# Kernel optimization log

Hardware: AMD Instinct MI355X
Metric: run time of the kernel (lower is better)

The kernel has to match this reference:

```python
import jax, jax.numpy as jnp
import numpy as np

N_TOKENS = 8192
IN_F = 4096
OUT_F = 4096
QMIN, QMAX = -128, 127  # get_quantized_range(8)
IN_SCALE = 0.02
OUT_SCALE = 0.05
IN_ZP = 0
OUT_ZP = 0


def setup_inputs() -> dict:
    key = jax.random.key(0)
    k1, k2, k3, k4 = jax.random.split(key, 4)
    x = jax.random.randint(k1, (N_TOKENS, IN_F), QMIN, QMAX + 1, dtype=jnp.int8)
    weight = jax.random.randint(k2, (OUT_F, IN_F), QMIN, QMAX + 1, dtype=jnp.int8)
    bias = jax.random.randint(k3, (OUT_F,), -1000, 1001, dtype=jnp.int32)
    weight_scale = jax.random.uniform(k4, (OUT_F, 1), dtype=jnp.float32, minval=0.005, maxval=0.02)
    return {"x": x, "weight": weight, "bias": bias, "weight_scale": weight_scale}


def reference(x, weight, bias, weight_scale):
    # int32-accumulated GEMM: [N, in] @ [in, out] + bias  (CPU path of the torch module)
    acc = jnp.matmul(x.astype(jnp.int32), weight.T.astype(jnp.int32)) + bias  # [N, out] int32
    ws = jnp.swapaxes(weight_scale, -1, -2)  # [1, out] per-output-channel scale
    out = acc.astype(jnp.float32) * (IN_SCALE * ws / OUT_SCALE)
    out = out + OUT_ZP
    out = jnp.clip(jnp.round(out), QMIN, QMAX).astype(jnp.int8)
    return out
```

## Files before the change

kernel.cpp:

```cpp
#include <hip/hip_runtime.h>
#include <hip/hip_bf16.h>
#include <stdint.h>

#define N_TOKENS 8192
#define IN_F 4096
#define OUT_F 4096

#define BM 256
#define BN 256
#define BKB 64
#define NKT (IN_F / BKB)

typedef int int32x4 __attribute__((ext_vector_type(4)));

__device__ __forceinline__ void gload_lds16(const signed char* g, signed char* lds) {
  __builtin_amdgcn_global_load_lds(
      (const __attribute__((address_space(1))) void*)g,
      (__attribute__((address_space(3))) void*)lds, 16, 0, 0);
}

__global__ void pack_kernel(const int4* __restrict__ xs, const int4* __restrict__ ws,
                            uchar4* __restrict__ xd, uchar4* __restrict__ wd,
                            int n4x, int n4tot) {
  const int stride = gridDim.x * blockDim.x;
  for (int i = blockIdx.x * blockDim.x + threadIdx.x; i < n4tot; i += stride) {
    int4 v;
    if (i < n4x) v = xs[i];
    else v = ws[i - n4x];
    uchar4 p;
    p.x = (unsigned char)(v.x & 255);
    p.y = (unsigned char)(v.y & 255);
    p.z = (unsigned char)(v.z & 255);
    p.w = (unsigned char)(v.w & 255);
    if (i < n4x) xd[i] = p;
    else wd[i - n4x] = p;
  }
}

__global__ __launch_bounds__(512, 2) void gemm_i8(
    const signed char* __restrict__ A, const signed char* __restrict__ B,
    const int* __restrict__ bias, const float* __restrict__ wscale,
    int* __restrict__ out) {
  __shared__ __align__(16) signed char sA[3][BM * BKB];
  __shared__ __align__(16) signed char sB[3][BN * BKB];

  const int tid = threadIdx.x;
  const int lane = tid & 63;
  const int w = tid >> 6;
  const int wr = w >> 2;
  const int wc = w & 3;

  const int brow = blockIdx.y * BM;
  const int bcol = blockIdx.x * BN;

  const int csrc = (((lane & 3) ^ ((lane >> 3) & 3)) << 4);
  const int r0 = w * 16 + (lane >> 2);
  const signed char* gA0 = A + (size_t)(brow + r0) * IN_F + csrc;
  const signed char* gB0 = B + (size_t)(bcol + r0) * IN_F + csrc;
  const int ldst = w * 1024 + lane * 16;

#define STAGE(tt, bf)                                                  \
  do {                                                                 \
    const size_t ko = (size_t)(tt)*BKB;                                \
    gload_lds16(gA0 + ko, &sA[bf][ldst]);                              \
    gload_lds16(gA0 + ko + (size_t)128 * IN_F, &sA[bf][ldst + 8192]);  \
    gload_lds16(gB0 + ko, &sB[bf][ldst]);                              \
    gload_lds16(gB0 + ko + (size_t)128 * IN_F, &sB[bf][ldst + 8192]);  \
  } while (0)

  const int cfrag = (((lane >> 4) ^ ((lane >> 1) & 3)) << 4);
  const int aoff = (wr * 128 + (lane & 15)) * BKB + cfrag;
  const int boff = (wc * 64 + (lane & 15)) * BKB + cfrag;

  int32x4 acc[8][4];
#pragma unroll
  for (int m = 0; m < 8; ++m)
#pragma unroll
    for (int n = 0; n < 4; ++n) acc[m][n] = (int32x4){0, 0, 0, 0};

  STAGE(0, 0);
  STAGE(1, 1);
  asm volatile("s_waitcnt vmcnt(4)" ::: "memory");
  __builtin_amdgcn_s_barrier();

  int bufR = 0, bufS = 2;
  for (int t = 0; t < NKT; ++t) {
    if (t < NKT - 2) STAGE(t + 2, bufS);

    int32x4 a[8], b[4];
#pragma unroll
    for (int n = 0; n < 4; ++n) b[n] = *(const int32x4*)&sB[bufR][boff + n * 1024];
#pragma unroll
    for (int m = 0; m < 4; ++m) a[m] = *(const int32x4*)&sA[bufR][aoff + m * 1024];
    __builtin_amdgcn_s_setprio(1);
#pragma unroll
    for (int m = 0; m < 4; ++m)
#pragma unroll
      for (int n = 0; n < 4; ++n)
        acc[m][n] = __builtin_amdgcn_mfma_i32_16x16x64_i8(a[m], b[n], acc[m][n], 0, 0, 0);
    __builtin_amdgcn_s_setprio(0);
    __builtin_amdgcn_s_barrier();
#pragma unroll
    for (int m = 4; m < 8; ++m) a[m] = *(const int32x4*)&sA[bufR][aoff + m * 1024];
    __builtin_amdgcn_s_setprio(1);
#pragma unroll
    for (int m = 4; m < 8; ++m)
#pragma unroll
      for (int n = 0; n < 4; ++n)
        acc[m][n] = __builtin_amdgcn_mfma_i32_16x16x64_i8(a[m], b[n], acc[m][n], 0, 0, 0);
    __builtin_amdgcn_s_setprio(0);

    if (t < NKT - 2) {
      asm volatile("s_waitcnt vmcnt(4) lgkmcnt(0)" ::: "memory");
      __builtin_amdgcn_s_barrier();
    } else if (t == NKT - 2) {
      asm volatile("s_waitcnt vmcnt(0) lgkmcnt(0)" ::: "memory");
      __builtin_amdgcn_s_barrier();
    }
    bufR = (bufR == 2) ? 0 : bufR + 1;
    bufS = (bufS == 2) ? 0 : bufS + 1;
  }
#undef STAGE

  const int colb = bcol + wc * 64 + (lane & 15);
  const int rowb = brow + wr * 128 + ((lane >> 4) << 2);
#pragma unroll
  for (int n = 0; n < 4; ++n) {
    const int col = colb + n * 16;
    const float s = 0.02f * wscale[col] / 0.05f;
    const int bz = bias[col];
#pragma unroll
    for (int m = 0; m < 8; ++m) {
      const int row0 = rowb + m * 16;
#pragma unroll
      for (int r = 0; r < 4; ++r) {
        float f = (float)(acc[m][n][r] + bz) * s;
        f = rintf(f);
        f = fminf(127.f, fmaxf(-128.f, f));
        out[(size_t)(row0 + r) * OUT_F + col] = (int)f;
      }
    }
  }
}

extern "C" void kernel_launch(void* const* d_in, const int* in_sizes, int n_in,
                              void* d_out, int out_size, void* d_ws, size_t ws_size,
                              hipStream_t stream) {
  const int* x = (const int*)d_in[0];
  const int* w = (const int*)d_in[1];
  const int* bias = (const int*)d_in[2];
  const float* wsc = (const float*)d_in[3];
  int* out = (int*)d_out;

  signed char* xp = (signed char*)d_ws;
  signed char* wp = xp + (size_t)N_TOKENS * IN_F;

  const int n4x = N_TOKENS * IN_F / 4;
  const int n4w = OUT_F * IN_F / 4;
  const int n4tot = n4x + n4w;

  pack_kernel<<<2048, 256, 0, stream>>>((const int4*)x, (const int4*)w,
                                        (uchar4*)xp, (uchar4*)wp, n4x, n4tot);

  dim3 grid(OUT_F / BN, N_TOKENS / BM);
  gemm_i8<<<grid, dim3(512), 0, stream>>>(xp, wp, bias, wsc, out);
}
```

Baseline: 442.0 us.

## Double K tile to 128 with two-buffer, four-phase interleaved load/MFMA pipeline

Raises the K tile from 64 to 128 bytes and replaces the triple-buffered LDS ring with double buffering. Each K iteration now runs four MFMA phases. The next tile's global-to-LDS loads are spread across those phases, and fine-grained vmcnt waits make sure each half of the tile is resident before it is read. This halves the number of loop iterations and spreads memory traffic between compute bursts. In exchange it adds more barriers per iteration, raises LDS use to 128KB, and the changed XOR swizzle and single prefetch stage may leave load latency less hidden.

```diff
diff --git a/kernel.cpp b/kernel.cpp
--- a/kernel.cpp
+++ b/kernel.cpp
@@ -8,7 +8,7 @@
 
 #define BM 256
 #define BN 256
-#define BKB 64
+#define BKB 128
 #define NKT (IN_F / BKB)
 
 typedef int int32x4 __attribute__((ext_vector_type(4)));
@@ -41,8 +41,8 @@
     const signed char* __restrict__ A, const signed char* __restrict__ B,
     const int* __restrict__ bias, const float* __restrict__ wscale,
     int* __restrict__ out) {
-  __shared__ __align__(16) signed char sA[3][BM * BKB];
-  __shared__ __align__(16) signed char sB[3][BN * BKB];
+  __shared__ __align__(16) signed char sA[2][BM * BKB];
+  __shared__ __align__(16) signed char sB[2][BN * BKB];
 
   const int tid = threadIdx.x;
   const int lane = tid & 63;
@@ -53,24 +53,17 @@
   const int brow = blockIdx.y * BM;
   const int bcol = blockIdx.x * BN;
 
-  const int csrc = (((lane & 3) ^ ((lane >> 3) & 3)) << 4);
-  const int r0 = w * 16 + (lane >> 2);
-  const signed char* gA0 = A + (size_t)(brow + r0) * IN_F + csrc;
-  const signed char* gB0 = B + (size_t)(bcol + r0) * IN_F + csrc;
-  const int ldst = w * 1024 + lane * 16;
-
-#define STAGE(tt, bf)                                                  \
-  do {                                                                 \
-    const size_t ko = (size_t)(tt)*BKB;                                \
-    gload_lds16(gA0 + ko, &sA[bf][ldst]);                              \
-    gload_lds16(gA0 + ko + (size_t)128 * IN_F, &sA[bf][ldst + 8192]);  \
-    gload_lds16(gB0 + ko, &sB[bf][ldst]);                              \
-    gload_lds16(gB0 + ko + (size_t)128 * IN_F, &sB[bf][ldst + 8192]);  \
-  } while (0)
-
-  const int cfrag = (((lane >> 4) ^ ((lane >> 1) & 3)) << 4);
-  const int aoff = (wr * 128 + (lane & 15)) * BKB + cfrag;
-  const int boff = (wc * 64 + (lane & 15)) * BKB + cfrag;
+  const int grow = tid >> 3;
+  const int gchk = ((tid & 7) ^ (grow & 7)) << 4;
+  const signed char* gA = A + (size_t)(brow + grow) * IN_F + gchk;
+  const signed char* gB = B + (size_t)(bcol + grow) * IN_F + gchk;
+  const int lst = tid << 4;
+#define GSTR ((size_t)64 * IN_F)
+
+  const int c0 = (((lane >> 4) ^ (lane & 7)) << 4);
+  const int c1 = c0 ^ 64;
+  const int rA = (wr * 128 + (lane & 15)) * BKB;
+  const int rB = (wc * 64 + (lane & 15)) * BKB;
 
   int32x4 acc[8][4];
 #pragma unroll
@@ -78,20 +71,32 @@
 #pragma unroll
     for (int n = 0; n < 4; ++n) acc[m][n] = (int32x4){0, 0, 0, 0};
 
-  STAGE(0, 0);
-  STAGE(1, 1);
-  asm volatile("s_waitcnt vmcnt(4)" ::: "memory");
+#pragma unroll
+  for (int i = 0; i < 4; ++i) {
+    gload_lds16(gB + i * GSTR, &sB[0][i * 8192 + lst]);
+    gload_lds16(gA + i * GSTR, &sA[0][i * 8192 + lst]);
+  }
+  asm volatile("s_waitcnt vmcnt(0)" ::: "memory");
   __builtin_amdgcn_s_barrier();
 
-  int bufR = 0, bufS = 2;
   for (int t = 0; t < NKT; ++t) {
-    if (t < NKT - 2) STAGE(t + 2, bufS);
-
-    int32x4 a[8], b[4];
-#pragma unroll
-    for (int n = 0; n < 4; ++n) b[n] = *(const int32x4*)&sB[bufR][boff + n * 1024];
-#pragma unroll
-    for (int m = 0; m < 4; ++m) a[m] = *(const int32x4*)&sA[bufR][aoff + m * 1024];
+    const int buf = t & 1;
+    const int nb = buf ^ 1;
+    const bool pf = (t < NKT - 1);
+    const signed char* srcA = gA + (size_t)(t + 1) * BKB;
+    const signed char* srcB = gB + (size_t)(t + 1) * BKB;
+    signed char* dA = &sA[nb][lst];
+    signed char* dB = &sB[nb][lst];
+    int32x4 a[4], b[4];
+
+#pragma unroll
+    for (int n = 0; n < 4; ++n) b[n] = *(const int32x4*)&sB[buf][rB + n * 2048 + c0];
+#pragma unroll
+    for (int m = 0; m < 4; ++m) a[m] = *(const int32x4*)&sA[buf][rA + m * 2048 + c0];
+    if (pf) { gload_lds16(srcB, dB); gload_lds16(srcB + 2 * GSTR, dB + 16384); }
+    __builtin_amdgcn_s_barrier();
+    asm volatile("s_waitcnt lgkmcnt(0)" ::: "memory");
+    __builtin_amdgcn_sched_barrier(0);
     __builtin_amdgcn_s_setprio(1);
 #pragma unroll
     for (int m = 0; m < 4; ++m)
@@ -99,28 +104,59 @@
       for (int n = 0; n < 4; ++n)
         acc[m][n] = __builtin_amdgcn_mfma_i32_16x16x64_i8(a[m], b[n], acc[m][n], 0, 0, 0);
     __builtin_amdgcn_s_setprio(0);
-    __builtin_amdgcn_s_barrier();
-#pragma unroll
-    for (int m = 4; m < 8; ++m) a[m] = *(const int32x4*)&sA[bufR][aoff + m * 1024];
-    __builtin_amdgcn_s_setprio(1);
-#pragma unroll
-    for (int m = 4; m < 8; ++m)
+    if (pf) asm volatile("s_waitcnt vmcnt(2)" ::: "memory");
+    else    asm volatile("s_waitcnt vmcnt(0)" ::: "memory");
+    __builtin_amdgcn_s_barrier();
+
+#pragma unroll
+    for (int m = 0; m < 4; ++m) a[m] = *(const int32x4*)&sA[buf][rA + (m + 4) * 2048 + c0];
+    if (pf) { gload_lds16(srcB + GSTR, dB + 8192); gload_lds16(srcB + 3 * GSTR, dB + 24576); }
+    __builtin_amdgcn_s_barrier();
+    asm volatile("s_waitcnt lgkmcnt(0)" ::: "memory");
+    __builtin_amdgcn_sched_barrier(0);
+    __builtin_amdgcn_s_setprio(1);
+#pragma unroll
+    for (int m = 0; m < 4; ++m)
+#pragma unroll
+      for (int n = 0; n < 4; ++n)
+        acc[m + 4][n] = __builtin_amdgcn_mfma_i32_16x16x64_i8(a[m], b[n], acc[m + 4][n], 0, 0, 0);
+    __builtin_amdgcn_s_setprio(0);
+    __builtin_amdgcn_s_barrier();
+
+#pragma unroll
+    for (int n = 0; n < 4; ++n) b[n] = *(const int32x4*)&sB[buf][rB + n * 2048 + c1];
+#pragma unroll
+    for (int m = 0; m < 4; ++m) a[m] = *(const int32x4*)&sA[buf][rA + m * 2048 + c1];
+    if (pf) { gload_lds16(srcA, dA); gload_lds16(srcA + 2 * GSTR, dA + 16384); }
+    __builtin_amdgcn_s_barrier();
+    asm volatile("s_waitcnt lgkmcnt(0)" ::: "memory");
+    __builtin_amdgcn_sched_barrier(0);
+    __builtin_amdgcn_s_setprio(1);
+#pragma unroll
+    for (int m = 0; m < 4; ++m)
 #pragma unroll
       for (int n = 0; n < 4; ++n)
         acc[m][n] = __builtin_amdgcn_mfma_i32_16x16x64_i8(a[m], b[n], acc[m][n], 0, 0, 0);
     __builtin_amdgcn_s_setprio(0);
-
-    if (t < NKT - 2) {
-      asm volatile("s_waitcnt vmcnt(4) lgkmcnt(0)" ::: "memory");
-      __builtin_amdgcn_s_barrier();
-    } else if (t == NKT - 2) {
-      asm volatile("s_waitcnt vmcnt(0) lgkmcnt(0)" ::: "memory");
-      __builtin_amdgcn_s_barrier();
-    }
-    bufR = (bufR == 2) ? 0 : bufR + 1;
-    bufS = (bufS == 2) ? 0 : bufS + 1;
-  }
-#undef STAGE
+    __builtin_amdgcn_s_barrier();
+
+#pragma unroll
+    for (int m = 0; m < 4; ++m) a[m] = *(const int32x4*)&sA[buf][rA + (m + 4) * 2048 + c1];
+    if (pf) { gload_lds16(srcA + GSTR, dA + 8192); gload_lds16(srcA + 3 * GSTR, dA + 24576); }
+    __builtin_amdgcn_s_barrier();
+    asm volatile("s_waitcnt lgkmcnt(0)" ::: "memory");
+    __builtin_amdgcn_sched_barrier(0);
+    __builtin_amdgcn_s_setprio(1);
+#pragma unroll
+    for (int m = 0; m < 4; ++m)
+#pragma unroll
+      for (int n = 0; n < 4; ++n)
+        acc[m + 4][n] = __builtin_amdgcn_mfma_i32_16x16x64_i8(a[m], b[n], acc[m + 4][n], 0, 0, 0);
+    __builtin_amdgcn_s_setprio(0);
+    asm volatile("s_waitcnt vmcnt(2)" ::: "memory");
+    __builtin_amdgcn_s_barrier();
+  }
+#undef GSTR
 
   const int colb = bcol + wc * 64 + (lane & 15);
   const int rowb = brow + wr * 128 + ((lane >> 4) << 2);
```

New measurement: 409.3 us. 1.08x faster.

## Deepen LDS pipeline to four buffers and interleave prefetch with MFMA phases

Applied to the files above, without the earlier changes.

Switches from triple to quad buffering with prefetch distance 3, and splits each k-step's global-to-LDS loads into B and A halves issued between the two MFMA phases. It also drops the XOR swizzle on LDS writes and reads in favour of a plain linear layout, and halves the A register fragment array. The aim is to hide more global memory latency and reduce register pressure. The trade-offs are more LDS per block (128KB), which may limit the two-blocks-per-CU occupancy, possible LDS bank conflicts from the removed swizzle, and extra barriers per iteration.

```diff
diff --git a/kernel.cpp b/kernel.cpp
--- a/kernel.cpp
+++ b/kernel.cpp
@@ -10,6 +10,7 @@
 #define BN 256
 #define BKB 64
 #define NKT (IN_F / BKB)
+#define NBUF 4
 
 typedef int int32x4 __attribute__((ext_vector_type(4)));
 
@@ -41,8 +42,8 @@
     const signed char* __restrict__ A, const signed char* __restrict__ B,
     const int* __restrict__ bias, const float* __restrict__ wscale,
     int* __restrict__ out) {
-  __shared__ __align__(16) signed char sA[3][BM * BKB];
-  __shared__ __align__(16) signed char sB[3][BN * BKB];
+  __shared__ __align__(16) signed char sA[NBUF][BM * BKB];
+  __shared__ __align__(16) signed char sB[NBUF][BN * BKB];
 
   const int tid = threadIdx.x;
   const int lane = tid & 63;
@@ -53,24 +54,14 @@
   const int brow = blockIdx.y * BM;
   const int bcol = blockIdx.x * BN;
 
-  const int csrc = (((lane & 3) ^ ((lane >> 3) & 3)) << 4);
-  const int r0 = w * 16 + (lane >> 2);
-  const signed char* gA0 = A + (size_t)(brow + r0) * IN_F + csrc;
-  const signed char* gB0 = B + (size_t)(bcol + r0) * IN_F + csrc;
-  const int ldst = w * 1024 + lane * 16;
+  const int grow = tid >> 2;
+  const signed char* gA = A + (size_t)(brow + grow) * IN_F + ((tid & 3) << 4);
+  const signed char* gB = B + (size_t)(bcol + grow) * IN_F + ((tid & 3) << 4);
+  const int lst = tid << 4;
+#define GSTR ((size_t)128 * IN_F)
 
-#define STAGE(tt, bf)                                                  \
-  do {                                                                 \
-    const size_t ko = (size_t)(tt)*BKB;                                \
-    gload_lds16(gA0 + ko, &sA[bf][ldst]);                              \
-    gload_lds16(gA0 + ko + (size_t)128 * IN_F, &sA[bf][ldst + 8192]);  \
-    gload_lds16(gB0 + ko, &sB[bf][ldst]);                              \
-    gload_lds16(gB0 + ko + (size_t)128 * IN_F, &sB[bf][ldst + 8192]);  \
-  } while (0)
-
-  const int cfrag = (((lane >> 4) ^ ((lane >> 1) & 3)) << 4);
-  const int aoff = (wr * 128 + (lane & 15)) * BKB + cfrag;
-  const int boff = (wc * 64 + (lane & 15)) * BKB + cfrag;
+  const int rA = (wr * 128 + (lane & 15)) * BKB + ((lane >> 4) << 4);
+  const int rB = (wc * 64 + (lane & 15)) * BKB + ((lane >> 4) << 4);
 
   int32x4 acc[8][4];
 #pragma unroll
@@ -78,20 +69,31 @@
 #pragma unroll
     for (int n = 0; n < 4; ++n) acc[m][n] = (int32x4){0, 0, 0, 0};
 
-  STAGE(0, 0);
-  STAGE(1, 1);
-  asm volatile("s_waitcnt vmcnt(4)" ::: "memory");
+#pragma unroll
+  for (int tt = 0; tt < 3; ++tt) {
+    gload_lds16(gB + tt * BKB, &sB[tt][lst]);
+    gload_lds16(gB + tt * BKB + GSTR, &sB[tt][8192 + lst]);
+    gload_lds16(gA + tt * BKB, &sA[tt][lst]);
+    gload_lds16(gA + tt * BKB + GSTR, &sA[tt][8192 + lst]);
+  }
+  asm volatile("s_waitcnt vmcnt(8)" ::: "memory");
   __builtin_amdgcn_s_barrier();
 
-  int bufR = 0, bufS = 2;
   for (int t = 0; t < NKT; ++t) {
-    if (t < NKT - 2) STAGE(t + 2, bufS);
+    const int buf = t & (NBUF - 1);
+    const int sbuf = (t + 3) & (NBUF - 1);
+    const bool pf = (t < NKT - 3);
+    const size_t so = (size_t)(t + 3) * BKB;
+    int32x4 a[4], b[4];
 
-    int32x4 a[8], b[4];
 #pragma unroll
-    for (int n = 0; n < 4; ++n) b[n] = *(const int32x4*)&sB[bufR][boff + n * 1024];
+    for (int n = 0; n < 4; ++n) b[n] = *(const int32x4*)&sB[buf][rB + n * 1024];
 #pragma unroll
-    for (int m = 0; m < 4; ++m) a[m] = *(const int32x4*)&sA[bufR][aoff + m * 1024];
+    for (int m = 0; m < 4; ++m) a[m] = *(const int32x4*)&sA[buf][rA + m * 1024];
+    if (pf) { gload_lds16(gB + so, &sB[sbuf][lst]); gload_lds16(gB + so + GSTR, &sB[sbuf][8192 + lst]); }
+    __builtin_amdgcn_s_barrier();
+    asm volatile("s_waitcnt lgkmcnt(0)" ::: "memory");
+    __builtin_amdgcn_sched_barrier(0);
     __builtin_amdgcn_s_setprio(1);
 #pragma unroll
     for (int m = 0; m < 4; ++m)
@@ -100,27 +102,33 @@
         acc[m][n] = __builtin_amdgcn_mfma_i32_16x16x64_i8(a[m], b[n], acc[m][n], 0, 0, 0);
     __builtin_amdgcn_s_setprio(0);
     __builtin_amdgcn_s_barrier();
+
 #pragma unroll
-    for (int m = 4; m < 8; ++m) a[m] = *(const int32x4*)&sA[bufR][aoff + m * 1024];
+    for (int m = 0; m < 4; ++m) a[m] = *(const int32x4*)&sA[buf][rA + (m + 4) * 1024];
+    if (pf) { gload_lds16(gA + so, &sA[sbuf][lst]); gload_lds16(gA + so + GSTR, &sA[sbuf][8192 + lst]); }
+    __builtin_amdgcn_s_barrier();
+    asm volatile("s_waitcnt lgkmcnt(0)" ::: "memory");
+    __builtin_amdgcn_sched_barrier(0);
     __builtin_amdgcn_s_setprio(1);
 #pragma unroll
-    for (int m = 4; m < 8; ++m)
+    for (int m = 0; m < 4; ++m)
 #pragma unroll
       for (int n = 0; n < 4; ++n)
-        acc[m][n] = __builtin_amdgcn_mfma_i32_16x16x64_i8(a[m], b[n], acc[m][n], 0, 0, 0);
+        acc[m + 4][n] = __builtin_amdgcn_mfma_i32_16x16x64_i8(a[m], b[n], acc[m + 4][n], 0, 0, 0);
     __builtin_amdgcn_s_setprio(0);
 
-    if (t < NKT - 2) {
-      asm volatile("s_waitcnt vmcnt(4) lgkmcnt(0)" ::: "memory");
+    if (t < NKT - 3) {
+      asm volatile("s_waitcnt vmcnt(8)" ::: "memory");
+      __builtin_amdgcn_s_barrier();
+    } else if (t == NKT - 3) {
+      asm volatile("s_waitcnt vmcnt(4)" ::: "memory");
       __builtin_amdgcn_s_barrier();
     } else if (t == NKT - 2) {
-      asm volatile("s_waitcnt vmcnt(0) lgkmcnt(0)" ::: "memory");
+      asm volatile("s_waitcnt vmcnt(0)" ::: "memory");
       __builtin_amdgcn_s_barrier();
     }
-    bufR = (bufR == 2) ? 0 : bufR + 1;
-    bufS = (bufS == 2) ? 0 : bufS + 1;
   }
-#undef STAGE
+#undef GSTR
 
   const int colb = bcol + wc * 64 + (lane & 15);
   const int rowb = brow + wr * 128 + ((lane >> 4) << 2);
```

Measured after the change: 411.6 us. -6.9%, faster.
